# Performance work log

Hardware: AMD Instinct MI355X
Metric: run time of the kernel (lower is better)

Reference implementation:

```python
import jax, jax.numpy as jnp
import numpy as np

S = 1024        # input sequence length
T = 512         # target_len
G = 1024        # number of history segments (len(history_count))
HTOT = 16384    # total history rows (sum of history_count)
LOC, TIM, CLU, UID = 50000, 48, 256, 2000
D_LOC, D_TIM, D_CLU, D_UID, HID = 512, 32, 64, 64, 512
INP = D_LOC + D_CLU + D_TIM  # 608


def setup_inputs() -> dict:
    key = jax.random.key(0)
    ks = jax.random.split(key, 20)
    f = lambda k, shape, scale=0.02: (jax.random.normal(k, shape, dtype=jnp.float32) * scale)
    cnt = HTOT // G
    return {
        "loc": jax.random.randint(ks[0], (S, 1), 0, LOC, dtype=jnp.int32),
        "tim": jax.random.randint(ks[1], (S, 1), 0, TIM, dtype=jnp.int32),
        "cluster": jax.random.randint(ks[2], (S, 1), 0, CLU, dtype=jnp.int32),
        "history_loc": jax.random.randint(ks[3], (HTOT, 1), 0, LOC, dtype=jnp.int32),
        "history_cluster": jax.random.randint(ks[4], (HTOT, 1), 0, CLU, dtype=jnp.int32),
        "history_tim": jax.random.randint(ks[5], (HTOT, 1), 0, TIM, dtype=jnp.int32),
        "history_count": jnp.full((G,), cnt, dtype=jnp.int32),
        "uid": jax.random.randint(ks[6], (1,), 0, UID, dtype=jnp.int32),
        "target_len": T,
        "emb_loc": f(ks[7], (LOC, D_LOC)),
        "emb_tim": f(ks[8], (TIM, D_TIM)),
        "emb_cluster": f(ks[9], (CLU, D_CLU)),
        "emb_uid": f(ks[10], (UID, D_UID)),
        "fc_attn_w": f(ks[11], (HID, INP)),
        "fc_attn_b": jnp.zeros((HID,), jnp.float32),
        "w_ih": f(ks[12], (3 * HID, INP)),
        "w_hh": f(ks[13], (3 * HID, HID)),
        "b_ih": jnp.zeros((3 * HID,), jnp.float32),
        "b_hh": jnp.zeros((3 * HID,), jnp.float32),
        "fc_final_w": f(ks[14], (LOC, 2 * HID + D_UID)),
        "fc_final_b": jnp.zeros((LOC,), jnp.float32),
    }


def _forward(loc, tim, cluster, history_loc, history_cluster, history_tim,
             history_count, uid, target_len,
             emb_loc, emb_tim, emb_cluster, emb_uid,
             fc_attn_w, fc_attn_b, w_ih, w_hh, b_ih, b_hh,
             fc_final_w, fc_final_b):
    # current trajectory embeddings -> x: [S, 1, INP]
    x = jnp.concatenate(
        [emb_loc[loc[:, 0]], emb_cluster[cluster[:, 0]], emb_tim[tim[:, 0]]], axis=-1
    )[:, None, :]

    # history embeddings (squeeze(1) in torch): [HTOT, D]
    h_loc = emb_loc[history_loc[:, 0]]
    h_clu = emb_cluster[history_cluster[:, 0]]
    h_tim = emb_tim[history_tim[:, 0]]

    # segment-mean pooling (replaces python loop over history_count)
    seg_ids = jnp.repeat(jnp.arange(G, dtype=jnp.int32), history_count,
                         total_repeat_length=HTOT)
    cnt_f = history_count.astype(h_loc.dtype)[:, None]
    loc_mean = jax.ops.segment_sum(h_loc, seg_ids, num_segments=G) / cnt_f
    clu_mean = jax.ops.segment_sum(h_clu, seg_ids, num_segments=G) / cnt_f
    offsets = jnp.concatenate([jnp.zeros((1,), jnp.int32),
                               jnp.cumsum(history_count)[:-1].astype(jnp.int32)])
    tim_first = h_tim[offsets]                       # [G, D_TIM]

    history = jnp.concatenate([loc_mean, clu_mean, tim_first], axis=1)  # [G, INP]
    history = jnp.tanh(history @ fc_attn_w.T + fc_attn_b)               # [G, HID]

    # GRU (PyTorch gate order r,z,n), batch=1, seq-major
    gx = jnp.einsum('sbi,gi->sbg', x, w_ih) + b_ih    # [S, 1, 3*HID]

    def step(h, gx_t):                                # h: [1, HID]
        gh = h @ w_hh.T + b_hh
        xr, xz, xn = jnp.split(gx_t, 3, axis=-1)
        hr, hz, hn = jnp.split(gh, 3, axis=-1)
        r = jax.nn.sigmoid(xr + hr)
        z = jax.nn.sigmoid(xz + hz)
        n = jnp.tanh(xn + r * hn)
        h_new = (1.0 - z) * n + z * h
        return h_new, h_new

    h0 = jnp.zeros((1, HID), x.dtype)
    _, outs = jax.lax.scan(step, h0, gx)              # [S, 1, HID]
    out_state = outs[:, 0, :]                         # [S, HID]

    q = out_state[-target_len:]                       # [T, HID]
    # dot attention: scores[i,j] = q_i . history_j, softmax over history
    attn = jax.nn.softmax(q @ history.T, axis=-1)     # [T, G]
    context = attn @ history                          # [T, HID]

    uid_emb = jnp.broadcast_to(emb_uid[uid[0]][None, :], (target_len, D_UID))
    out = jnp.concatenate([q, context, uid_emb], axis=1)  # [T, 2*HID+D_UID]
    y = out @ fc_final_w.T + fc_final_b               # [T, LOC]
    return jax.nn.log_softmax(y, axis=-1)


def reference(loc, tim, cluster, history_loc, history_cluster, history_tim,
              history_count, uid, target_len,
              emb_loc, emb_tim, emb_cluster, emb_uid,
              fc_attn_w, fc_attn_b, w_ih, w_hh, b_ih, b_hh,
              fc_final_w, fc_final_b):
    return _forward(loc, tim, cluster, history_loc, history_cluster, history_tim,
                    history_count, uid, target_len,
                    emb_loc, emb_tim, emb_cluster, emb_uid,
                    fc_attn_w, fc_attn_b, w_ih, w_hh, b_ih, b_hh,
                    fc_final_w, fc_final_b)
```

## Files before the change

### kernel.cpp

```cpp
#include <hip/hip_runtime.h>
#include <hip/hip_bf16.h>
#include <math.h>

#define S_LEN 1024
#define T_LEN 512
#define G_NUM 1024
#define NLOC  50000
#define HID   512
#define INP   608
#define OUTD  1088
#define GRU_WGS 32

typedef float f32x4 __attribute__((ext_vector_type(4)));
typedef short bf16x8 __attribute__((ext_vector_type(8)));

__global__ __launch_bounds__(1024) void k_init(const int* counts, int* offs) {
    __shared__ int sh[1024];
    int tid = threadIdx.x;
    sh[tid] = counts[tid];
    __syncthreads();
    for (int st = 1; st < 1024; st <<= 1) {
        int v = (tid >= st) ? sh[tid - st] : 0;
        __syncthreads();
        sh[tid] += v;
        __syncthreads();
    }
    offs[tid] = sh[tid] - counts[tid];
}

__global__ __launch_bounds__(256) void k_feats(
    const int* __restrict__ hloc, const int* __restrict__ hclu,
    const int* __restrict__ htim, const int* __restrict__ counts,
    const int* __restrict__ offs,
    const float* __restrict__ emb_loc, const float* __restrict__ emb_clu,
    const float* __restrict__ emb_tim, float* __restrict__ feats) {
    int g = blockIdx.x, tid = threadIdx.x;
    __shared__ int iloc[64], iclu[64];
    __shared__ int itim0;
    int off = offs[g], cn = counts[g];
    if (tid < cn) { iloc[tid] = hloc[off + tid]; iclu[tid] = hclu[off + tid]; }
    if (tid == 0) itim0 = htim[off];
    __syncthreads();
    float inv = 1.0f / (float)cn;
    for (int d = tid; d < 512; d += 256) {
        float s = 0.f;
        for (int i = 0; i < cn; ++i) s += emb_loc[iloc[i] * 512 + d];
        feats[g * INP + d] = s * inv;
    }
    for (int d = tid; d < 64; d += 256) {
        float s = 0.f;
        for (int i = 0; i < cn; ++i) s += emb_clu[iclu[i] * 64 + d];
        feats[g * INP + 512 + d] = s * inv;
    }
    for (int d = tid; d < 32; d += 256)
        feats[g * INP + 576 + d] = emb_tim[itim0 * 32 + d];
}

__global__ __launch_bounds__(256) void k_xfeat(
    const int* __restrict__ loc, const int* __restrict__ clu,
    const int* __restrict__ tim,
    const float* __restrict__ emb_loc, const float* __restrict__ emb_clu,
    const float* __restrict__ emb_tim, float* __restrict__ x) {
    int s = blockIdx.x, tid = threadIdx.x;
    int il = loc[s], ic = clu[s], it = tim[s];
    for (int d = tid; d < 512; d += 256) x[s * INP + d] = emb_loc[il * 512 + d];
    for (int d = tid; d < 64; d += 256) x[s * INP + 512 + d] = emb_clu[ic * 64 + d];
    for (int d = tid; d < 32; d += 256) x[s * INP + 576 + d] = emb_tim[it * 32 + d];
}

__global__ __launch_bounds__(256) void k_gemm8(
    const float* __restrict__ A, const float* __restrict__ W,
    const float* __restrict__ bias, float* __restrict__ out,
    int ldout, int act) {
    __shared__ float ash[8][INP];
    int r0 = blockIdx.x * 8, c0 = blockIdx.y * 512;
    int tid = threadIdx.x;
    for (int i = tid; i < 8 * INP; i += 256)
        ash[i / INP][i % INP] = A[(r0 + i / INP) * INP + (i % INP)];
    __syncthreads();
    for (int cc = 0; cc < 2; ++cc) {
        int c = c0 + cc * 256 + tid;
        float acc[8];
#pragma unroll
        for (int r = 0; r < 8; ++r) acc[r] = 0.f;
        const float* wr = &W[(long)c * INP];
        for (int k = 0; k < INP; k += 4) {
            float4 wv = *(const float4*)&wr[k];
#pragma unroll
            for (int r = 0; r < 8; ++r) {
                float4 av = *(const float4*)&ash[r][k];
                acc[r] += av.x * wv.x + av.y * wv.y + av.z * wv.z + av.w * wv.w;
            }
        }
#pragma unroll
        for (int r = 0; r < 8; ++r) {
            float v = acc[r] + bias[c];
            if (act) v = tanhf(v);
            out[(long)(r0 + r) * ldout + c] = v;
        }
    }
}

__global__ __launch_bounds__(256, 1) void k_gru(
    const float* __restrict__ w_hh, const float* __restrict__ b_hh,
    const float* __restrict__ gx, unsigned long long* __restrict__ tb,
    float* __restrict__ outmat) {
    __shared__ float hsh[512];
    const int wg = blockIdx.x, tid = threadIdx.x;
    const int grp = tid >> 4, lane = tid & 15;
    const int j = wg * 16 + grp;

    float4 wr[8], wz[8], wn[8];
#pragma unroll
    for (int m = 0; m < 8; ++m) {
        wr[m] = *(const float4*)&w_hh[(long)(0 * 512 + j) * 512 + m * 64 + lane * 4];
        wz[m] = *(const float4*)&w_hh[(long)(1 * 512 + j) * 512 + m * 64 + lane * 4];
        wn[m] = *(const float4*)&w_hh[(long)(2 * 512 + j) * 512 + m * 64 + lane * 4];
    }
    const float bhr = b_hh[j], bhz = b_hh[512 + j], bhn = b_hh[1024 + j];
    hsh[tid] = 0.f; hsh[tid + 256] = 0.f;
    __syncthreads();

    for (int t = 0; t < S_LEN; ++t) {
        float xr = gx[t * 1536 + j];
        float xz = gx[t * 1536 + 512 + j];
        float xn = gx[t * 1536 + 1024 + j];
        if (t > 0) {
            const unsigned int want = (unsigned int)(t - 1);
            const unsigned long long* b = tb + (((t - 1) & 1) << 9);
            unsigned long long v0 = __hip_atomic_load(b + tid, __ATOMIC_RELAXED,
                                                      __HIP_MEMORY_SCOPE_AGENT);
            while ((unsigned int)(v0 >> 32) != want)
                v0 = __hip_atomic_load(b + tid, __ATOMIC_RELAXED,
                                       __HIP_MEMORY_SCOPE_AGENT);
            unsigned long long v1 = __hip_atomic_load(b + tid + 256, __ATOMIC_RELAXED,
                                                      __HIP_MEMORY_SCOPE_AGENT);
            while ((unsigned int)(v1 >> 32) != want)
                v1 = __hip_atomic_load(b + tid + 256, __ATOMIC_RELAXED,
                                       __HIP_MEMORY_SCOPE_AGENT);
            hsh[tid] = __uint_as_float((unsigned int)v0);
            hsh[tid + 256] = __uint_as_float((unsigned int)v1);
        }
        __syncthreads();
        float sr = 0.f, sz = 0.f, sn = 0.f;
#pragma unroll
        for (int m = 0; m < 8; ++m) {
            float4 hv = *(const float4*)&hsh[m * 64 + lane * 4];
            sr += wr[m].x * hv.x + wr[m].y * hv.y + wr[m].z * hv.z + wr[m].w * hv.w;
            sz += wz[m].x * hv.x + wz[m].y * hv.y + wz[m].z * hv.z + wz[m].w * hv.w;
            sn += wn[m].x * hv.x + wn[m].y * hv.y + wn[m].z * hv.z + wn[m].w * hv.w;
        }
#pragma unroll
        for (int off = 8; off; off >>= 1) {
            sr += __shfl_xor(sr, off);
            sz += __shfl_xor(sz, off);
            sn += __shfl_xor(sn, off);
        }
        if (lane == 0) {
            float r = 1.f / (1.f + __expf(-(xr + sr + bhr)));
            float z = 1.f / (1.f + __expf(-(xz + sz + bhz)));
            float n = tanhf(xn + r * (sn + bhn));
            float hold = hsh[j];
            float hnew = (1.f - z) * n + z * hold;
            unsigned long long pk =
                ((unsigned long long)(unsigned int)t << 32) | __float_as_uint(hnew);
            __hip_atomic_store(tb + ((t & 1) << 9) + j, pk, __ATOMIC_RELAXED,
                               __HIP_MEMORY_SCOPE_AGENT);
            if (t >= S_LEN - T_LEN) outmat[(t - (S_LEN - T_LEN)) * OUTD + j] = hnew;
        }
        __syncthreads();
    }
}

__global__ __launch_bounds__(256) void k_attn(
    const float* __restrict__ history, const float* __restrict__ emb_uid,
    const int* __restrict__ uid, float* __restrict__ outmat) {
    __shared__ float qsh[8][512];
    __shared__ float psh[8][1024];
    __shared__ float sc[4];
    int r0 = blockIdx.x * 8, tid = threadIdx.x;
    for (int i = tid; i < 8 * 512; i += 256)
        qsh[i >> 9][i & 511] = outmat[(r0 + (i >> 9)) * OUTD + (i & 511)];
    __syncthreads();
    for (int cc = 0; cc < 4; ++cc) {
        int g = cc * 256 + tid;
        float acc[8];
#pragma unroll
        for (int r = 0; r < 8; ++r) acc[r] = 0.f;
        const float* hrow = &history[g * 512];
        for (int k = 0; k < 512; k += 4) {
            float4 hv = *(const float4*)&hrow[k];
#pragma unroll
            for (int r = 0; r < 8; ++r) {
                float4 qv = *(const float4*)&qsh[r][k];
                acc[r] += qv.x * hv.x + qv.y * hv.y + qv.z * hv.z + qv.w * hv.w;
            }
        }
#pragma unroll
        for (int r = 0; r < 8; ++r) psh[r][g] = acc[r];
    }
    __syncthreads();
    for (int r = 0; r < 8; ++r) {
        float m = -1e30f;
        for (int cc = 0; cc < 4; ++cc) m = fmaxf(m, psh[r][cc * 256 + tid]);
#pragma unroll
        for (int off = 32; off; off >>= 1) m = fmaxf(m, __shfl_xor(m, off));
        if ((tid & 63) == 0) sc[tid >> 6] = m;
        __syncthreads();
        m = fmaxf(fmaxf(sc[0], sc[1]), fmaxf(sc[2], sc[3]));
        __syncthreads();
        float ss = 0.f;
        for (int cc = 0; cc < 4; ++cc) {
            int g = cc * 256 + tid;
            float e = __expf(psh[r][g] - m);
            psh[r][g] = e;
            ss += e;
        }
#pragma unroll
        for (int off = 32; off; off >>= 1) ss += __shfl_xor(ss, off);
        if ((tid & 63) == 0) sc[tid >> 6] = ss;
        __syncthreads();
        ss = sc[0] + sc[1] + sc[2] + sc[3];
        float inv = 1.f / ss;
        for (int cc = 0; cc < 4; ++cc) psh[r][cc * 256 + tid] *= inv;
        __syncthreads();
    }
    for (int dd = 0; dd < 2; ++dd) {
        int d = dd * 256 + tid;
        float acc[8];
#pragma unroll
        for (int r = 0; r < 8; ++r) acc[r] = 0.f;
        for (int g = 0; g < 1024; ++g) {
            float hv = history[g * 512 + d];
#pragma unroll
            for (int r = 0; r < 8; ++r) acc[r] += psh[r][g] * hv;
        }
#pragma unroll
        for (int r = 0; r < 8; ++r) outmat[(r0 + r) * OUTD + 512 + d] = acc[r];
    }
    int u = uid[0];
    for (int i = tid; i < 8 * 64; i += 256)
        outmat[(r0 + (i >> 6)) * OUTD + 1024 + (i & 63)] = emb_uid[u * 64 + (i & 63)];
}

__global__ __launch_bounds__(256) void k_cvt(const float* __restrict__ in,
                                             __hip_bfloat16* __restrict__ out, int n) {
    int i = blockIdx.x * 256 + threadIdx.x;
    if (i < n) out[i] = __float2bfloat16(in[i]);
}

__global__ __launch_bounds__(256, 2) void k_final(
    const __hip_bfloat16* __restrict__ Abf, const float* __restrict__ Wf,
    const float* __restrict__ bias, float* __restrict__ y) {
    __shared__ __hip_bfloat16 ash[512 * 40];
    __shared__ __hip_bfloat16 bsh[64 * 40];
    const int n0 = blockIdx.x * 64;
    const int tid = threadIdx.x;
    const int wave = tid >> 6, lane = tid & 63;
    f32x4 acc[32];
#pragma unroll
    for (int i = 0; i < 32; ++i) acc[i] = (f32x4){0.f, 0.f, 0.f, 0.f};

    for (int kc = 0; kc < 34; ++kc) {
        const int k0 = kc * 32;
        __syncthreads();
#pragma unroll
        for (int rr = 0; rr < 2; ++rr) {
            int r = tid + rr * 256;
            const uint4* src = (const uint4*)(Abf + r * OUTD + k0);
            uint4 v0 = src[0], v1 = src[1], v2 = src[2], v3 = src[3];
            uint4* dst = (uint4*)(ash + r * 40);
            dst[0] = v0; dst[1] = v1; dst[2] = v2; dst[3] = v3;
        }
        {
            int rb = tid >> 2, q = tid & 3;
            int n = n0 + rb;
            float4 w0 = {0.f, 0.f, 0.f, 0.f}, w1 = {0.f, 0.f, 0.f, 0.f};
            if (n < NLOC) {
                const float4* wsrc = (const float4*)(Wf + (long)n * OUTD + k0 + q * 8);
                w0 = wsrc[0]; w1 = wsrc[1];
            }
            __hip_bfloat16* bd = bsh + rb * 40 + q * 8;
            bd[0] = __float2bfloat16(w0.x); bd[1] = __float2bfloat16(w0.y);
            bd[2] = __float2bfloat16(w0.z); bd[3] = __float2bfloat16(w0.w);
            bd[4] = __float2bfloat16(w1.x); bd[5] = __float2bfloat16(w1.y);
            bd[6] = __float2bfloat16(w1.z); bd[7] = __float2bfloat16(w1.w);
        }
        __syncthreads();
        const int nlane = lane & 15, quad = lane >> 4;
        bf16x8 bfrag = *(const bf16x8*)(bsh + (wave * 16 + nlane) * 40 + quad * 8);
#pragma unroll
        for (int mt = 0; mt < 32; ++mt) {
            bf16x8 afrag = *(const bf16x8*)(ash + (mt * 16 + nlane) * 40 + quad * 8);
            acc[mt] = __builtin_amdgcn_mfma_f32_16x16x32_bf16(afrag, bfrag, acc[mt], 0, 0, 0);
        }
    }
    const int nlane = lane & 15, quad = lane >> 4;
    const int col = n0 + wave * 16 + nlane;
    if (col < NLOC) {
        float bv = bias[col];
#pragma unroll
        for (int mt = 0; mt < 32; ++mt) {
            int rbase = mt * 16 + quad * 4;
#pragma unroll
            for (int i = 0; i < 4; ++i)
                y[(rbase + i) * NLOC + col] = acc[mt][i] + bv;
        }
    }
}

__global__ __launch_bounds__(256) void k_lse(const float* __restrict__ y,
                                             float* __restrict__ lse) {
    __shared__ float sm[4], ssb[4];
    int row = blockIdx.x, tid = threadIdx.x;
    const float* rp = y + (long)row * NLOC;
    float m = -1e30f, s = 0.f;
    for (int i = tid * 4; i < NLOC; i += 1024) {
        float4 v = *(const float4*)&rp[i];
        float mv = fmaxf(fmaxf(v.x, v.y), fmaxf(v.z, v.w));
        if (mv > m) { s *= __expf(m - mv); m = mv; }
        s += __expf(v.x - m) + __expf(v.y - m) + __expf(v.z - m) + __expf(v.w - m);
    }
#pragma unroll
    for (int off = 32; off; off >>= 1) {
        float om = __shfl_xor(m, off), os = __shfl_xor(s, off);
        float nm = fmaxf(m, om);
        s = s * __expf(m - nm) + os * __expf(om - nm);
        m = nm;
    }
    if ((tid & 63) == 0) { sm[tid >> 6] = m; ssb[tid >> 6] = s; }
    __syncthreads();
    if (tid == 0) {
        float M = sm[0], SS = ssb[0];
        for (int i = 1; i < 4; ++i) {
            float nm = fmaxf(M, sm[i]);
            SS = SS * __expf(M - nm) + ssb[i] * __expf(sm[i] - nm);
            M = nm;
        }
        lse[row] = M + logf(SS);
    }
}

__global__ __launch_bounds__(256) void k_sub(float* __restrict__ y,
                                             const float* __restrict__ lse) {
    int i4 = blockIdx.x * 256 + threadIdx.x;
    int row = i4 / 12500;
    float l = lse[row];
    float4* p = (float4*)y + i4;
    float4 v = *p;
    v.x -= l; v.y -= l; v.z -= l; v.w -= l;
    *p = v;
}

extern "C" void kernel_launch(void* const* d_in, const int* in_sizes, int n_in,
                              void* d_out, int out_size, void* d_ws, size_t ws_size,
                              hipStream_t stream) {
    const int* loc  = (const int*)d_in[0];
    const int* tim  = (const int*)d_in[1];
    const int* clu  = (const int*)d_in[2];
    const int* hloc = (const int*)d_in[3];
    const int* hclu = (const int*)d_in[4];
    const int* htim = (const int*)d_in[5];
    const int* hcnt = (const int*)d_in[6];
    const int* uid  = (const int*)d_in[7];
    const float* emb_loc    = (const float*)d_in[9];
    const float* emb_tim    = (const float*)d_in[10];
    const float* emb_clu    = (const float*)d_in[11];
    const float* emb_uid    = (const float*)d_in[12];
    const float* fc_attn_w  = (const float*)d_in[13];
    const float* fc_attn_b  = (const float*)d_in[14];
    const float* w_ih       = (const float*)d_in[15];
    const float* w_hh       = (const float*)d_in[16];
    const float* b_ih       = (const float*)d_in[17];
    const float* b_hh       = (const float*)d_in[18];
    const float* fc_final_w = (const float*)d_in[19];
    const float* fc_final_b = (const float*)d_in[20];
    float* y = (float*)d_out;

    float* feats  = (float*)d_ws;
    float* xf     = feats + G_NUM * INP;
    float* hist   = xf + S_LEN * INP;
    float* gx     = hist + G_NUM * HID;
    float* outmat = gx + S_LEN * 1536;
    float* lse    = outmat + T_LEN * OUTD;
    unsigned long long* tb = (unsigned long long*)(lse + T_LEN);
    __hip_bfloat16* outbf = (__hip_bfloat16*)(tb + 2 * 512);
    int* offs = (int*)((char*)outbf + (size_t)T_LEN * OUTD * 2);

    k_init<<<1, 1024, 0, stream>>>(hcnt, offs);
    k_feats<<<G_NUM, 256, 0, stream>>>(hloc, hclu, htim, hcnt, offs,
                                       emb_loc, emb_clu, emb_tim, feats);
    k_xfeat<<<S_LEN, 256, 0, stream>>>(loc, clu, tim, emb_loc, emb_clu, emb_tim, xf);
    k_gemm8<<<dim3(G_NUM / 8, 1), 256, 0, stream>>>(feats, fc_attn_w, fc_attn_b,
                                                    hist, HID, 1);
    k_gemm8<<<dim3(S_LEN / 8, 3), 256, 0, stream>>>(xf, w_ih, b_ih, gx, 1536, 0);
    k_gru<<<GRU_WGS, 256, 0, stream>>>(w_hh, b_hh, gx, tb, outmat);
    k_attn<<<T_LEN / 8, 256, 0, stream>>>(hist, emb_uid, uid, outmat);
    k_cvt<<<(T_LEN * OUTD + 255) / 256, 256, 0, stream>>>(outmat, outbf, T_LEN * OUTD);
    k_final<<<(NLOC + 63) / 64, 256, 0, stream>>>(outbf, fc_final_w, fc_final_b, y);
    k_lse<<<T_LEN, 256, 0, stream>>>(y, lse);
    k_sub<<<(T_LEN * (NLOC / 4)) / 256, 256, 0, stream>>>(y, lse);
}
```

Before: 3.475 ms.

## Restructure persistent GRU kernel: 512 threads, single-wave polling, double-buffered hidden state

The persistent GRU kernel now uses 512 threads per block with 32 lanes per hidden unit, which halves the per-thread register-resident weights and adds one more shuffle-reduction stage. Polling of the global step buffer moves to a single wavefront that issues 8 loads up front, re-polls with s_sleep, and only reloads entries that are still pending. The shared hidden state is double-buffered by step parity, so the trailing barrier at the end of each step can be dropped. The aim is to cut per-step synchronisation latency on the serial recurrence, which dominates total time, at the cost of extra reduction work and sleep-induced polling delay.

```diff
diff --git a/kernel.cpp b/kernel.cpp
--- a/kernel.cpp
+++ b/kernel.cpp
@@ -101,57 +101,75 @@
     }
 }
 
-__global__ __launch_bounds__(256, 1) void k_gru(
+__global__ __launch_bounds__(512, 2) void k_gru(
     const float* __restrict__ w_hh, const float* __restrict__ b_hh,
     const float* __restrict__ gx, unsigned long long* __restrict__ tb,
     float* __restrict__ outmat) {
-    __shared__ float hsh[512];
+    __shared__ float hsh[2][512];
     const int wg = blockIdx.x, tid = threadIdx.x;
-    const int grp = tid >> 4, lane = tid & 15;
+    const int grp = tid >> 5, lane = tid & 31;
     const int j = wg * 16 + grp;
 
-    float4 wr[8], wz[8], wn[8];
-#pragma unroll
-    for (int m = 0; m < 8; ++m) {
-        wr[m] = *(const float4*)&w_hh[(long)(0 * 512 + j) * 512 + m * 64 + lane * 4];
-        wz[m] = *(const float4*)&w_hh[(long)(1 * 512 + j) * 512 + m * 64 + lane * 4];
-        wn[m] = *(const float4*)&w_hh[(long)(2 * 512 + j) * 512 + m * 64 + lane * 4];
+    float4 wr[4], wz[4], wn[4];
+#pragma unroll
+    for (int m = 0; m < 4; ++m) {
+        wr[m] = *(const float4*)&w_hh[(long)(0 * 512 + j) * 512 + m * 128 + lane * 4];
+        wz[m] = *(const float4*)&w_hh[(long)(1 * 512 + j) * 512 + m * 128 + lane * 4];
+        wn[m] = *(const float4*)&w_hh[(long)(2 * 512 + j) * 512 + m * 128 + lane * 4];
     }
     const float bhr = b_hh[j], bhz = b_hh[512 + j], bhn = b_hh[1024 + j];
-    hsh[tid] = 0.f; hsh[tid + 256] = 0.f;
+    hsh[0][tid] = 0.f;
     __syncthreads();
 
     for (int t = 0; t < S_LEN; ++t) {
-        float xr = gx[t * 1536 + j];
-        float xz = gx[t * 1536 + 512 + j];
-        float xn = gx[t * 1536 + 1024 + j];
-        if (t > 0) {
+        float xr = 0.f, xz = 0.f, xn = 0.f;
+        if (lane == 0) {
+            xr = gx[t * 1536 + j];
+            xz = gx[t * 1536 + 512 + j];
+            xn = gx[t * 1536 + 1024 + j];
+        }
+        if (t > 0 && tid < 64) {
             const unsigned int want = (unsigned int)(t - 1);
             const unsigned long long* b = tb + (((t - 1) & 1) << 9);
-            unsigned long long v0 = __hip_atomic_load(b + tid, __ATOMIC_RELAXED,
-                                                      __HIP_MEMORY_SCOPE_AGENT);
-            while ((unsigned int)(v0 >> 32) != want)
-                v0 = __hip_atomic_load(b + tid, __ATOMIC_RELAXED,
-                                       __HIP_MEMORY_SCOPE_AGENT);
-            unsigned long long v1 = __hip_atomic_load(b + tid + 256, __ATOMIC_RELAXED,
-                                                      __HIP_MEMORY_SCOPE_AGENT);
-            while ((unsigned int)(v1 >> 32) != want)
-                v1 = __hip_atomic_load(b + tid + 256, __ATOMIC_RELAXED,
-                                       __HIP_MEMORY_SCOPE_AGENT);
-            hsh[tid] = __uint_as_float((unsigned int)v0);
-            hsh[tid + 256] = __uint_as_float((unsigned int)v1);
-        }
-        __syncthreads();
+            unsigned long long v[8];
+            int ok = 0;
+#pragma unroll
+            for (int i = 0; i < 8; ++i)
+                v[i] = __hip_atomic_load(b + tid + i * 64, __ATOMIC_RELAXED,
+                                         __HIP_MEMORY_SCOPE_AGENT);
+            for (;;) {
+                int pend = 0;
+#pragma unroll
+                for (int i = 0; i < 8; ++i) {
+                    if (!(ok & (1 << i))) {
+                        if ((unsigned int)(v[i] >> 32) == want) {
+                            ok |= (1 << i);
+                            hsh[t & 1][tid + i * 64] =
+                                __uint_as_float((unsigned int)v[i]);
+                        } else pend = 1;
+                    }
+                }
+                if (!pend) break;
+                __builtin_amdgcn_s_sleep(1);
+#pragma unroll
+                for (int i = 0; i < 8; ++i)
+                    if (!(ok & (1 << i)))
+                        v[i] = __hip_atomic_load(b + tid + i * 64, __ATOMIC_RELAXED,
+                                                 __HIP_MEMORY_SCOPE_AGENT);
+            }
+        }
+        __syncthreads();
+        const float* hp = hsh[t & 1];
         float sr = 0.f, sz = 0.f, sn = 0.f;
 #pragma unroll
-        for (int m = 0; m < 8; ++m) {
-            float4 hv = *(const float4*)&hsh[m * 64 + lane * 4];
+        for (int m = 0; m < 4; ++m) {
+            float4 hv = *(const float4*)&hp[m * 128 + lane * 4];
             sr += wr[m].x * hv.x + wr[m].y * hv.y + wr[m].z * hv.z + wr[m].w * hv.w;
             sz += wz[m].x * hv.x + wz[m].y * hv.y + wz[m].z * hv.z + wz[m].w * hv.w;
             sn += wn[m].x * hv.x + wn[m].y * hv.y + wn[m].z * hv.z + wn[m].w * hv.w;
         }
 #pragma unroll
-        for (int off = 8; off; off >>= 1) {
+        for (int off = 16; off; off >>= 1) {
             sr += __shfl_xor(sr, off);
             sz += __shfl_xor(sz, off);
             sn += __shfl_xor(sn, off);
@@ -160,15 +178,13 @@
             float r = 1.f / (1.f + __expf(-(xr + sr + bhr)));
             float z = 1.f / (1.f + __expf(-(xz + sz + bhz)));
             float n = tanhf(xn + r * (sn + bhn));
-            float hold = hsh[j];
-            float hnew = (1.f - z) * n + z * hold;
+            float hnew = (1.f - z) * n + z * hp[j];
             unsigned long long pk =
                 ((unsigned long long)(unsigned int)t << 32) | __float_as_uint(hnew);
             __hip_atomic_store(tb + ((t & 1) << 9) + j, pk, __ATOMIC_RELAXED,
                                __HIP_MEMORY_SCOPE_AGENT);
             if (t >= S_LEN - T_LEN) outmat[(t - (S_LEN - T_LEN)) * OUTD + j] = hnew;
         }
-        __syncthreads();
     }
 }
 
@@ -394,7 +410,7 @@
     k_gemm8<<<dim3(G_NUM / 8, 1), 256, 0, stream>>>(feats, fc_attn_w, fc_attn_b,
                                                     hist, HID, 1);
     k_gemm8<<<dim3(S_LEN / 8, 3), 256, 0, stream>>>(xf, w_ih, b_ih, gx, 1536, 0);
-    k_gru<<<GRU_WGS, 256, 0, stream>>>(w_hh, b_hh, gx, tb, outmat);
+    k_gru<<<GRU_WGS, 512, 0, stream>>>(w_hh, b_hh, gx, tb, outmat);
     k_attn<<<T_LEN / 8, 256, 0, stream>>>(hist, emb_uid, uid, outmat);
     k_cvt<<<(T_LEN * OUTD + 255) / 256, 256, 0, stream>>>(outmat, outbf, T_LEN * OUTD);
     k_final<<<(NLOC + 63) / 64, 256, 0, stream>>>(outbf, fc_final_w, fc_final_b, y);
```

After: 3.532 ms. No clear change (+1.6%).
